# Kernel optimization log

Measured on AMD Instinct MI355X. Metric: run time of the kernel, lower is better.

## Reference

```python
import jax, jax.numpy as jnp
import numpy as np
from jax import lax

B, T, SLEN = 65536, 512, 12

def setup_inputs() -> dict:
    key = jax.random.key(0)
    k0, k1, k2 = jax.random.split(key, 3)
    series = jax.random.normal(k0, (B, T), dtype=jnp.float32)
    series_shifts = jax.random.randint(k1, (B,), 0, SLEN)
    init_season = jax.random.uniform(k2, (SLEN,), dtype=jnp.float32)
    return {
        'series': series,
        'series_shifts': series_shifts,
        'alpha': jnp.asarray(0.1, jnp.float32),
        'beta': jnp.asarray(0.1, jnp.float32),
        'gamma': jnp.asarray(0.1, jnp.float32),
        'init_season': init_season,
        'init_trend': jnp.asarray(0.1, jnp.float32),
        'n_preds': 0,  # only runnable value (original code indexes series[:, i] for all i)
    }


def reference(series, series_shifts, alpha, beta, gamma, init_season, init_trend, n_preds):
    # series: (B, T) float32; series_shifts: (B,) int roll amounts
    b, t = series.shape
    slen = init_season.shape[0]
    # Per-batch rolled initial seasonals, as in torch.roll(init_season, shift)
    rolled = jax.vmap(lambda r: jnp.roll(init_season, r))(series_shifts)  # (B, slen)
    # In the original code seasonals[i % slen] always reads the INITIAL rolled
    # seasonal (appended gamma-updates live at indices >= slen and are never read),
    # so the seasonal sequence is fully determined up-front.
    seas = rolled[:, jnp.arange(t) % slen]  # (B, T)

    smooth0 = series[:, 0]                              # (B,)
    trend0 = jnp.full((b,), init_trend, series.dtype)   # (B,)
    res0 = smooth0 + trend0                             # i == 0 output (no seasonal)

    def step(carry, x):
        smooth, trend = carry
        y, season_prev = x  # series[:, i], seasonal at i % slen
        smooth_new = alpha * (y - season_prev) + (1.0 - alpha) * (smooth + trend)
        trend_new = beta * (smooth_new - smooth) + (1.0 - beta) * trend
        res = smooth_new + trend_new + season_prev
        return (smooth_new, trend_new), res

    xs = (series[:, 1:].T, seas[:, 1:].T)  # (T-1, B) each
    _, res_rest = lax.scan(step, (smooth0, trend0), xs)  # (T-1, B)
    result = jnp.concatenate([res0[None, :], res_rest], axis=0).T  # (B, T)
    # n_preds == 0: original returns result[:, -0:] == full series
    return result if n_preds == 0 else result[:, -n_preds:]
```

## Files before the change

### kernel.cpp

```cpp
#include <hip/hip_runtime.h>

#define NB 65536
#define NT 512
#define SLEN 12
#define BLOCK 256
#define TCOLS 32
#define NTILE (NT / TCOLS)
#define LSTRIDE 36

__global__ __launch_bounds__(BLOCK) void holtwinters_kernel(
    const float* __restrict__ series,
    const int*   __restrict__ shifts,
    const float* __restrict__ alpha_p,
    const float* __restrict__ beta_p,
    const float* __restrict__ init_season,
    const float* __restrict__ trend0_p,
    float*       __restrict__ out)
{
    __shared__ float ss[SLEN];
    __shared__ __align__(16) float tile[BLOCK * LSTRIDE];

    if (threadIdx.x < SLEN) ss[threadIdx.x] = init_season[threadIdx.x];

    const int t    = threadIdx.x;
    const int row0 = blockIdx.x * BLOCK;
    const int b    = row0 + t;

    const float alpha  = alpha_p[0];
    const float beta   = beta_p[0];
    const float oma    = 1.0f - alpha;
    const float omb    = 1.0f - beta;
    const float trend0 = trend0_p[0];

    const int shift = shifts[b];
    int sidx = (SLEN - (shift % SLEN)) % SLEN;

    const int lrow = t >> 3;
    const int lcol = (t & 7) * 4;

    float4 nxt[8];
    #pragma unroll
    for (int j = 0; j < 8; ++j) {
        const int r = j * 32 + lrow;
        nxt[j] = *(const float4*)(series + (size_t)(row0 + r) * NT + lcol);
    }

    float smooth = 0.0f, trend = 0.0f;
    __syncthreads();

    for (int c = 0; c < NTILE; ++c) {
        #pragma unroll
        for (int j = 0; j < 8; ++j) {
            const int r = j * 32 + lrow;
            *(float4*)&tile[r * LSTRIDE + lcol] = nxt[j];
        }
        __syncthreads();

        if (c + 1 < NTILE) {
            #pragma unroll
            for (int j = 0; j < 8; ++j) {
                const int r = j * 32 + lrow;
                nxt[j] = *(const float4*)(series + (size_t)(row0 + r) * NT
                                          + (c + 1) * TCOLS + lcol);
            }
        }

        float v[TCOLS];
        #pragma unroll
        for (int q = 0; q < 8; ++q) {
            const float4 rd = *(const float4*)&tile[t * LSTRIDE + 4 * q];
            v[4*q+0] = rd.x; v[4*q+1] = rd.y; v[4*q+2] = rd.z; v[4*q+3] = rd.w;
        }
        #pragma unroll
        for (int k = 0; k < TCOLS; ++k) {
            const float s = ss[sidx];
            sidx = (sidx + 1 == SLEN) ? 0 : sidx + 1;
            const float y = v[k];
            if (k == 0 && c == 0) {
                smooth = y;
                trend  = trend0;
                v[0]   = smooth + trend;
            } else {
                const float st = smooth + trend;
                const float sm = alpha * (y - s) + oma * st;
                trend  = beta * (sm - smooth) + omb * trend;
                smooth = sm;
                v[k]   = sm + trend + s;
            }
        }
        #pragma unroll
        for (int q = 0; q < 8; ++q) {
            *(float4*)&tile[t * LSTRIDE + 4 * q] =
                make_float4(v[4*q+0], v[4*q+1], v[4*q+2], v[4*q+3]);
        }
        __syncthreads();

        #pragma unroll
        for (int j = 0; j < 8; ++j) {
            const int r = j * 32 + lrow;
            const float4 wv = *(const float4*)&tile[r * LSTRIDE + lcol];
            *(float4*)(out + (size_t)(row0 + r) * NT + c * TCOLS + lcol) = wv;
        }
        __syncthreads();
    }
}

extern "C" void kernel_launch(void* const* d_in, const int* in_sizes, int n_in,
                              void* d_out, int out_size, void* d_ws, size_t ws_size,
                              hipStream_t stream) {
    const float* series      = (const float*)d_in[0];
    const int*   shifts      = (const int*)  d_in[1];
    const float* alpha       = (const float*)d_in[2];
    const float* beta        = (const float*)d_in[3];
    const float* init_season = (const float*)d_in[5];
    const float* init_trend  = (const float*)d_in[6];
    float*       out         = (float*)d_out;

    dim3 block(BLOCK);
    dim3 grid(NB / BLOCK);
    hipLaunchKernelGGL(holtwinters_kernel, grid, block, 0, stream,
                       series, shifts, alpha, beta, init_season, init_trend, out);
}
```

Before: 265.7 us.

## Parallelize time recurrence via chunked linear scan with matrix-power carry fixup

```diff
diff --git a/kernel.cpp b/kernel.cpp
--- a/kernel.cpp
+++ b/kernel.cpp
@@ -4,9 +4,12 @@
 #define NT 512
 #define SLEN 12
 #define BLOCK 256
-#define TCOLS 32
-#define NTILE (NT / TCOLS)
-#define LSTRIDE 36
+#define ROWS 8
+#define CHUNKS 32
+#define CLEN 16
+#define CSTR 20
+#define ROWSTR (CHUNKS * CSTR)
+#define YSZ (ROWS * ROWSTR)
 
 __global__ __launch_bounds__(BLOCK) void holtwinters_kernel(
     const float* __restrict__ series,
@@ -17,14 +20,15 @@
     const float* __restrict__ trend0_p,
     float*       __restrict__ out)
 {
-    __shared__ float ss[SLEN];
-    __shared__ __align__(16) float tile[BLOCK * LSTRIDE];
-
-    if (threadIdx.x < SLEN) ss[threadIdx.x] = init_season[threadIdx.x];
+    __shared__ __align__(16) float  y[YSZ];
+    __shared__ float2 endst[ROWS * CHUNKS];
+    __shared__ float2 sarr [ROWS * CHUNKS];
+    __shared__ float2 u[CLEN + 1];
+    __shared__ float  Mm[4];
+    __shared__ float  ss[SLEN];
 
     const int t    = threadIdx.x;
-    const int row0 = blockIdx.x * BLOCK;
-    const int b    = row0 + t;
+    const int row0 = blockIdx.x * ROWS;
 
     const float alpha  = alpha_p[0];
     const float beta   = beta_p[0];
@@ -32,76 +36,121 @@
     const float omb    = 1.0f - beta;
     const float trend0 = trend0_p[0];
 
-    const int shift = shifts[b];
-    int sidx = (SLEN - (shift % SLEN)) % SLEN;
+    if (t < SLEN) ss[t] = init_season[t];
 
-    const int lrow = t >> 3;
-    const int lcol = (t & 7) * 4;
-
-    float4 nxt[8];
-    #pragma unroll
-    for (int j = 0; j < 8; ++j) {
-        const int r = j * 32 + lrow;
-        nxt[j] = *(const float4*)(series + (size_t)(row0 + r) * NT + lcol);
+    if (t == 0) {
+        const float a00 = oma, a01 = oma;
+        const float a10 = -alpha * beta, a11 = beta * oma + omb;
+        float p0 = 1.0f, p1 = 1.0f;
+        for (int j = 1; j <= CLEN; ++j) {
+            const float q0 = p0 * a00 + p1 * a10;
+            const float q1 = p0 * a01 + p1 * a11;
+            p0 = q0; p1 = q1;
+            u[j] = make_float2(p0, p1);
+        }
+        float m00 = a00, m01 = a01, m10 = a10, m11 = a11;
+        for (int sq = 0; sq < 4; ++sq) {
+            const float n00 = m00 * m00 + m01 * m10;
+            const float n01 = m00 * m01 + m01 * m11;
+            const float n10 = m10 * m00 + m11 * m10;
+            const float n11 = m10 * m01 + m11 * m11;
+            m00 = n00; m01 = n01; m10 = n10; m11 = n11;
+        }
+        Mm[0] = m00; Mm[1] = m01; Mm[2] = m10; Mm[3] = m11;
     }
 
-    float smooth = 0.0f, trend = 0.0f;
+    {
+        const float4* __restrict__ src = (const float4*)(series + (size_t)row0 * NT);
+        #pragma unroll
+        for (int i = 0; i < 4; ++i) {
+            const int g   = t + i * BLOCK;
+            const int r   = g >> 7;
+            const int col = (g & 127) * 4;
+            const int c   = col >> 4, k = col & 15;
+            const float4 v = src[g];
+            *(float4*)&y[r * ROWSTR + c * CSTR + k] = v;
+        }
+    }
     __syncthreads();
 
-    for (int c = 0; c < NTILE; ++c) {
+    const int r = t >> 5;
+    const int c = t & 31;
+    const int shift = shifts[row0 + r];
+    int sidx = ((c * CLEN - shift) % SLEN + SLEN) % SLEN;
+
+    float o[CLEN];
+    float smooth = 0.0f, trend = 0.0f;
+    {
+        const float* yb = &y[r * ROWSTR + c * CSTR];
         #pragma unroll
-        for (int j = 0; j < 8; ++j) {
-            const int r = j * 32 + lrow;
-            *(float4*)&tile[r * LSTRIDE + lcol] = nxt[j];
-        }
-        __syncthreads();
-
-        if (c + 1 < NTILE) {
+        for (int q = 0; q < 4; ++q) {
+            const float4 yv = *(const float4*)(yb + 4 * q);
+            const float ya[4] = {yv.x, yv.y, yv.z, yv.w};
             #pragma unroll
-            for (int j = 0; j < 8; ++j) {
-                const int r = j * 32 + lrow;
-                nxt[j] = *(const float4*)(series + (size_t)(row0 + r) * NT
-                                          + (c + 1) * TCOLS + lcol);
+            for (int kk = 0; kk < 4; ++kk) {
+                const int k = 4 * q + kk;
+                const float s = ss[sidx];
+                sidx = (sidx + 1 == SLEN) ? 0 : sidx + 1;
+                const float yy = ya[kk];
+                if (c == 0 && k == 0) {
+                    smooth = yy;
+                    trend  = trend0;
+                    o[0]   = smooth + trend;
+                } else {
+                    const float st = smooth + trend;
+                    const float sm = alpha * (yy - s) + oma * st;
+                    trend  = beta * (sm - smooth) + omb * trend;
+                    smooth = sm;
+                    o[k]   = sm + trend + s;
+                }
             }
         }
+    }
+    endst[t] = make_float2(smooth, trend);
+    __syncthreads();
 
-        float v[TCOLS];
+    if (c == 0) {
+        const float m00 = Mm[0], m01 = Mm[1], m10 = Mm[2], m11 = Mm[3];
+        float2 e0 = endst[r * CHUNKS + 0];
+        float Sx = e0.x, Sy = e0.y;
+        sarr[r * CHUNKS + 1] = make_float2(Sx, Sy);
+        for (int cc = 2; cc < CHUNKS; ++cc) {
+            const float2 rr = endst[r * CHUNKS + cc - 1];
+            const float nx = m00 * Sx + m01 * Sy + rr.x;
+            const float ny = m10 * Sx + m11 * Sy + rr.y;
+            Sx = nx; Sy = ny;
+            sarr[r * CHUNKS + cc] = make_float2(Sx, Sy);
+        }
+    }
+    __syncthreads();
+
+    if (c != 0) {
+        const float2 S = sarr[r * CHUNKS + c];
         #pragma unroll
-        for (int q = 0; q < 8; ++q) {
-            const float4 rd = *(const float4*)&tile[t * LSTRIDE + 4 * q];
-            v[4*q+0] = rd.x; v[4*q+1] = rd.y; v[4*q+2] = rd.z; v[4*q+3] = rd.w;
+        for (int k = 0; k < CLEN; ++k) {
+            const float2 uk = u[k + 1];
+            o[k] += uk.x * S.x + uk.y * S.y;
         }
+    }
+    {
+        float* yb = &y[r * ROWSTR + c * CSTR];
         #pragma unroll
-        for (int k = 0; k < TCOLS; ++k) {
-            const float s = ss[sidx];
-            sidx = (sidx + 1 == SLEN) ? 0 : sidx + 1;
-            const float y = v[k];
-            if (k == 0 && c == 0) {
-                smooth = y;
-                trend  = trend0;
-                v[0]   = smooth + trend;
-            } else {
-                const float st = smooth + trend;
-                const float sm = alpha * (y - s) + oma * st;
-                trend  = beta * (sm - smooth) + omb * trend;
-                smooth = sm;
-                v[k]   = sm + trend + s;
-            }
+        for (int q = 0; q < 4; ++q)
+            *(float4*)(yb + 4 * q) =
+                make_float4(o[4*q], o[4*q+1], o[4*q+2], o[4*q+3]);
+    }
+    __syncthreads();
+
+    {
+        float4* __restrict__ dst = (float4*)(out + (size_t)row0 * NT);
+        #pragma unroll
+        for (int i = 0; i < 4; ++i) {
+            const int g   = t + i * BLOCK;
+            const int rr  = g >> 7;
+            const int col = (g & 127) * 4;
+            const int cc  = col >> 4, kk = col & 15;
+            dst[g] = *(const float4*)&y[rr * ROWSTR + cc * CSTR + kk];
         }
-        #pragma unroll
-        for (int q = 0; q < 8; ++q) {
-            *(float4*)&tile[t * LSTRIDE + 4 * q] =
-                make_float4(v[4*q+0], v[4*q+1], v[4*q+2], v[4*q+3]);
-        }
-        __syncthreads();
-
-        #pragma unroll
-        for (int j = 0; j < 8; ++j) {
-            const int r = j * 32 + lrow;
-            const float4 wv = *(const float4*)&tile[r * LSTRIDE + lcol];
-            *(float4*)(out + (size_t)(row0 + r) * NT + c * TCOLS + lcol) = wv;
-        }
-        __syncthreads();
     }
 }
 
@@ -117,7 +166,7 @@
     float*       out         = (float*)d_out;
 
     dim3 block(BLOCK);
-    dim3 grid(NB / BLOCK);
+    dim3 grid(NB / ROWS);
     hipLaunchKernelGGL(holtwinters_kernel, grid, block, 0, stream,
                        series, shifts, alpha, beta, init_season, init_trend, out);
 }
```

Measured after the change: 241.4 us. 1.1x faster.
